# Optimization experiments

Measured on AMD Instinct MI355X. Metric: run time of the kernel, lower is better.

The kernel has to match this reference:

```python
import jax, jax.numpy as jnp
import numpy as np

ND, PD, NH = 256, 128, 8   # node_dim, pair_dim, n_head
HD = ND // NH              # head_dim = 32
N, L = 1, 256


def _inorm(x):
    # InstanceNorm2d (affine=False), x is NHWC: normalize per (N,C) over H,W
    m = jnp.mean(x, axis=(1, 2), keepdims=True)
    v = jnp.var(x, axis=(1, 2), keepdims=True)
    return (x - m) * jax.lax.rsqrt(v + 1e-5)


def _conv3x3(x, w, b):
    # w in torch OIHW layout -> HWIO; stride 1, padding 1 ('SAME')
    y = jax.lax.conv_general_dilated(x, jnp.transpose(w, (2, 3, 1, 0)), (1, 1), 'SAME',
                                     dimension_numbers=('NHWC', 'HWIO', 'NHWC'))
    return y + b


def _lrelu(x):
    return jnp.where(x >= 0, x, 0.01 * x)


def _ln(x, g, b):
    m = jnp.mean(x, axis=-1, keepdims=True)
    v = jnp.var(x, axis=-1, keepdims=True)
    return (x - m) * jax.lax.rsqrt(v + 1e-5) * g + b


def setup_inputs() -> dict:
    key = jax.random.key(0)
    ks = jax.random.split(key, 16)
    rn = lambda k, s: jax.random.normal(k, s, jnp.float32) * 0.02
    return dict(
        x=jax.random.normal(ks[0], (N, L, ND), jnp.float32),
        z=jax.random.normal(ks[1], (N, L, L, PD), jnp.float32),
        plddt=jax.random.uniform(ks[2], (N, L, L, 1), jnp.float32),
        Wq=rn(ks[3], (ND, ND)), Wk=rn(ks[4], (ND, ND)), Wv=rn(ks[5], (ND, ND)),
        Wp2a=rn(ks[6], (NH, PD)),
        conv_a_w=rn(ks[7], (NH, 2 * NH, 3, 3)), conv_a_b=jnp.zeros((NH,), jnp.float32),
        conv_p_w=rn(ks[8], (NH, NH + 1, 3, 3)), conv_p_b=jnp.zeros((NH,), jnp.float32),
        ln1_g=jnp.ones((NH * PD + ND,), jnp.float32), ln1_b=jnp.zeros((NH * PD + ND,), jnp.float32),
        lin1_w=rn(ks[9], (2 * ND, NH * PD + ND)), lin1_b=jnp.zeros((2 * ND,), jnp.float32),
        ln2_g=jnp.ones((2 * ND,), jnp.float32), ln2_b=jnp.zeros((2 * ND,), jnp.float32),
        lin2_w=rn(ks[10], (ND, 2 * ND)), lin2_b=jnp.zeros((ND,), jnp.float32),
        lnf_g=jnp.ones((ND,), jnp.float32), lnf_b=jnp.zeros((ND,), jnp.float32),
        conv_z_w=rn(ks[11], (PD, NH + PD, 3, 3)), conv_z_b=jnp.zeros((PD,), jnp.float32),
    )


def reference(x, z, plddt, Wq, Wk, Wv, Wp2a, conv_a_w, conv_a_b, conv_p_w, conv_p_b,
              ln1_g, ln1_b, lin1_w, lin1_b, ln2_g, ln2_b, lin2_w, lin2_b,
              lnf_g, lnf_b, conv_z_w, conv_z_b):
    n, l, _ = x.shape
    inv_sqrt_hd = np.float32(1.0 / np.sqrt(HD))
    # _node2alpha: per-head QK^T / sqrt(head_dim) -> (N,L,L,H)
    q = (x @ Wq.T).reshape(n, l, NH, HD)
    k = (x @ Wk.T).reshape(n, l, NH, HD)
    v = (x @ Wv.T).reshape(n, l, NH, HD)
    a_node = jnp.einsum('nihd,njhd->nijh', q, k) * inv_sqrt_hd
    # _pair2alpha
    a_pair = z @ Wp2a.T  # (N,L,L,H)
    # conv2dalpha: cat(pair, node) channels-last, InstanceNorm + Conv3x3 + LeakyReLU
    alpha = _lrelu(_conv3x3(_inorm(jnp.concatenate([a_pair, a_node], axis=-1)), conv_a_w, conv_a_b))
    # alpha_mask_plddt
    alpha = _lrelu(_conv3x3(_inorm(jnp.concatenate([alpha, plddt], axis=-1)), conv_p_w, conv_p_b))
    # _node_aggregation: (N,L,H,hd) head-major flatten -> (N,L,node_dim)
    node_from_node = jnp.einsum('nijh,njhd->nihd', alpha, v).reshape(n, l, ND)
    # _pair_aggregation: direct contraction over j (avoids (N,L,L,H,P) blowup)
    node_from_pair = jnp.einsum('nijh,nijp->nihp', alpha, z).reshape(n, l, NH * PD)
    # out_transform: LN -> Linear -> LN -> LeakyReLU -> Linear
    h = jnp.concatenate([node_from_pair, node_from_node], axis=-1)
    h = _ln(h, ln1_g, ln1_b)
    h = _ln(h @ lin1_w.T + lin1_b, ln2_g, ln2_b)
    x_out = _lrelu(h) @ lin2_w.T + lin2_b
    x_new = _ln(x + x_out, lnf_g, lnf_b)
    # alpha2pair
    z_new = _lrelu(_conv3x3(_inorm(jnp.concatenate([z, alpha], axis=-1)), conv_z_w, conv_z_b))
    return x_new, z_new
```

## Files before the change

### kernel.cpp

```cpp
#include <hip/hip_runtime.h>
#include <math.h>

#define LLEN 256
#define NDIM 256
#define NHEAD 8
#define HDIM 32
#define NPIX (LLEN*LLEN)

typedef __bf16 bf16x8 __attribute__((ext_vector_type(8)));
typedef float f32x4 __attribute__((ext_vector_type(4)));

constexpr size_t OFF_Q     = 0;
constexpr size_t OFF_K     = 65536;
constexpr size_t OFF_V     = 131072;
constexpr size_t OFF_CAT16 = 196608;
constexpr size_t OFF_H1B   = 196608;
constexpr size_t OFF_W1B   = 360448;
constexpr size_t OFF_A1    = 1245184;
constexpr size_t OFF_ALPHA = 1769472;
constexpr size_t OFF_AGG   = 2293760;
constexpr size_t OFF_Y     = 2621440;
constexpr size_t OFF_ST16  = 2752512;
constexpr size_t OFF_ST9   = 2752544;
constexpr size_t OFF_ST136 = 2752576;
constexpr size_t OFF_PART  = 2752864;
constexpr size_t OFF_PART2 = 2892128;
constexpr size_t OFF_WZB2  = 3031392;

__device__ inline unsigned short f2b(float x){
  union { float f; unsigned u; } a; a.f = x;
  unsigned r = a.u + 0x7fffu + ((a.u >> 16) & 1u);
  return (unsigned short)(r >> 16);
}

__global__ __launch_bounds__(256) void qkv_kernel(
    const float* __restrict__ x, const float* __restrict__ Wq,
    const float* __restrict__ Wk, const float* __restrict__ Wv,
    float* __restrict__ q, float* __restrict__ k, float* __restrict__ v){
  __shared__ __align__(16) float xs[8][256];
  int t = threadIdx.x;
  int i0 = blockIdx.x * 8;
  int m = blockIdx.y;
  const float* W = (m==0)?Wq:((m==1)?Wk:Wv);
  float* out = (m==0)?q:((m==1)?k:v);
  for (int idx = t; idx < 2048; idx += 256)
    xs[idx>>8][idx&255] = x[(size_t)i0*256 + idx];
  __syncthreads();
  float acc[8];
  #pragma unroll
  for (int r = 0; r < 8; r++) acc[r] = 0.f;
  const float4* wr = (const float4*)(W + (size_t)t*256);
  for (int kk = 0; kk < 64; ++kk){
    float4 w4 = wr[kk];
    #pragma unroll
    for (int r = 0; r < 8; r++){
      float4 xv = ((const float4*)xs[r])[kk];
      acc[r] += w4.x*xv.x + w4.y*xv.y + w4.z*xv.z + w4.w*xv.w;
    }
  }
  #pragma unroll
  for (int r = 0; r < 8; r++) out[(size_t)(i0+r)*256 + t] = acc[r];
}

__global__ __launch_bounds__(256) void cat16v2_kernel(
    const float* __restrict__ z, const float* __restrict__ qb,
    const float* __restrict__ kb, const float* __restrict__ Wp2a,
    float* __restrict__ cat16){
  __shared__ __align__(16) float zs2[32*132];
  __shared__ __align__(16) float ws2[8*132];
  __shared__ __align__(16) float qs2[8*36];
  __shared__ __align__(16) float ks2[32*288];
  int t = threadIdx.x;
  int pix0 = blockIdx.x * 32;
  int i = pix0 >> 8;
  int j0 = pix0 & 255;
  {
    int h = t >> 5, j = t & 31;
    float4 v = *(const float4*)(Wp2a + h*128 + j*4);
    *(float4*)(ws2 + h*132 + j*4) = v;
  }
  if (t < 64){
    int h = t >> 3, d4 = t & 7;
    float4 v = *(const float4*)(qb + (size_t)i*256 + h*32 + d4*4);
    *(float4*)(qs2 + h*36 + d4*4) = v;
  }
  #pragma unroll
  for (int k = 0; k < 4; ++k){
    int idx = t + k*256;
    int pix = idx >> 5, j = idx & 31;
    float4 v = *(const float4*)(z + ((size_t)(pix0 + pix))*128 + j*4);
    *(float4*)(zs2 + pix*132 + j*4) = v;
  }
  #pragma unroll
  for (int k = 0; k < 8; ++k){
    int idx = t + k*256;
    int pix = idx >> 6, rem = idx & 63, h = rem >> 3, d4 = rem & 7;
    float4 v = *(const float4*)(kb + ((size_t)(j0 + pix))*256 + h*32 + d4*4);
    *(float4*)(ks2 + pix*288 + h*36 + d4*4) = v;
  }
  __syncthreads();
  int p8 = t >> 3, h = t & 7;
  const float* zr = zs2 + p8*132;
  const float* wr = ws2 + h*132;
  float ap = 0.f;
  #pragma unroll 8
  for (int j = 0; j < 32; ++j){
    float4 a = *(const float4*)(zr + j*4);
    float4 b = *(const float4*)(wr + j*4);
    ap += a.x*b.x + a.y*b.y + a.z*b.z + a.w*b.w;
  }
  const float* qr = qs2 + h*36;
  const float* kr = ks2 + p8*288 + h*36;
  float an = 0.f;
  #pragma unroll
  for (int d4 = 0; d4 < 8; ++d4){
    float4 a = *(const float4*)(qr + d4*4);
    float4 b = *(const float4*)(kr + d4*4);
    an += a.x*b.x + a.y*b.y + a.z*b.z + a.w*b.w;
  }
  an *= 0.17677669529663689f;
  int pix = pix0 + p8;
  cat16[(size_t)pix*16 + h] = ap;
  cat16[(size_t)pix*16 + 8 + h] = an;
}

__global__ __launch_bounds__(256) void statsA_z_kernel(
    const float* __restrict__ z, float* __restrict__ part, float* __restrict__ part2){
  __shared__ float4 sm[256], sq[256];
  int t = threadIdx.x, b = blockIdx.x;
  int c4 = t & 31, po = t >> 5;
  float4 s = {0,0,0,0}, q = {0,0,0,0};
  for (int g = 0; g < 8; ++g){
    int px = b*64 + po + g*8;
    float4 v = *(const float4*)(z + (size_t)px*128 + c4*4);
    s.x += v.x; s.y += v.y; s.z += v.z; s.w += v.w;
    q.x += v.x*v.x; q.y += v.y*v.y; q.z += v.z*v.z; q.w += v.w*v.w;
  }
  sm[t] = s; sq[t] = q;
  __syncthreads();
  if (t < 32){
    float4 S = sm[t], Q = sq[t];
    for (int p2 = 1; p2 < 8; ++p2){
      float4 a = sm[p2*32 + t], c = sq[p2*32 + t];
      S.x += a.x; S.y += a.y; S.z += a.z; S.w += a.w;
      Q.x += c.x; Q.y += c.y; Q.z += c.z; Q.w += c.w;
    }
    part [(size_t)(t*4+0)*1024 + b] = S.x; part [(size_t)(t*4+1)*1024 + b] = S.y;
    part [(size_t)(t*4+2)*1024 + b] = S.z; part [(size_t)(t*4+3)*1024 + b] = S.w;
    part2[(size_t)(t*4+0)*1024 + b] = Q.x; part2[(size_t)(t*4+1)*1024 + b] = Q.y;
    part2[(size_t)(t*4+2)*1024 + b] = Q.z; part2[(size_t)(t*4+3)*1024 + b] = Q.w;
  }
}

__global__ __launch_bounds__(256) void statsA_16_kernel(
    const float* __restrict__ src, float* __restrict__ part, float* __restrict__ part2){
  __shared__ float4 sm[256], sq[256];
  int t = threadIdx.x, b = blockIdx.x;
  int c4 = t & 3, po = t >> 2;
  float4 s = {0,0,0,0}, q = {0,0,0,0};
  for (int g = 0; g < 4; ++g){
    int px = b*256 + po + g*64;
    float4 v = *(const float4*)(src + (size_t)px*16 + c4*4);
    s.x += v.x; s.y += v.y; s.z += v.z; s.w += v.w;
    q.x += v.x*v.x; q.y += v.y*v.y; q.z += v.z*v.z; q.w += v.w*v.w;
  }
  sm[t] = s; sq[t] = q;
  __syncthreads();
  if (t < 4){
    float4 S = sm[t], Q = sq[t];
    for (int p2 = 1; p2 < 64; ++p2){
      float4 a = sm[p2*4 + t], c = sq[p2*4 + t];
      S.x += a.x; S.y += a.y; S.z += a.z; S.w += a.w;
      Q.x += c.x; Q.y += c.y; Q.z += c.z; Q.w += c.w;
    }
    part [(size_t)(t*4+0)*1024 + b] = S.x; part [(size_t)(t*4+1)*1024 + b] = S.y;
    part [(size_t)(t*4+2)*1024 + b] = S.z; part [(size_t)(t*4+3)*1024 + b] = S.w;
    part2[(size_t)(t*4+0)*1024 + b] = Q.x; part2[(size_t)(t*4+1)*1024 + b] = Q.y;
    part2[(size_t)(t*4+2)*1024 + b] = Q.z; part2[(size_t)(t*4+3)*1024 + b] = Q.w;
  }
}

__global__ __launch_bounds__(256) void statsA_s8_kernel(
    const float* __restrict__ src, float* __restrict__ part, float* __restrict__ part2,
    int coff){
  __shared__ float sm[256], sq[256];
  int t = threadIdx.x, b = blockIdx.x;
  int ch = t & 7, po = t >> 3;
  float s = 0.f, q = 0.f;
  for (int g = 0; g < 8; ++g){
    int px = b*256 + po + g*32;
    float v = src[(size_t)px*8 + ch];
    s += v; q += v*v;
  }
  sm[t] = s; sq[t] = q;
  __syncthreads();
  if (t < 8){
    float S = 0.f, Q = 0.f;
    for (int p2 = 0; p2 < 32; ++p2){ S += sm[p2*8 + t]; Q += sq[p2*8 + t]; }
    part [(size_t)(coff+t)*1024 + b] = S;
    part2[(size_t)(coff+t)*1024 + b] = Q;
  }
}

__device__ inline void block_reduce2(float& s, float& s2, float* red){
  int t = threadIdx.x;
  int lane = t & 63, wv = t >> 6;
  #pragma unroll
  for (int o = 32; o > 0; o >>= 1){ s += __shfl_down(s, o); s2 += __shfl_down(s2, o); }
  __syncthreads();
  if (lane == 0){ red[wv] = s; red[4+wv] = s2; }
  __syncthreads();
  s  = red[0]+red[1]+red[2]+red[3];
  s2 = red[4]+red[5]+red[6]+red[7];
}

__global__ __launch_bounds__(256) void statsA_s1_kernel(
    const float* __restrict__ src, float* __restrict__ part, float* __restrict__ part2,
    int coff){
  __shared__ float red[8];
  int t = threadIdx.x, b = blockIdx.x;
  float v = src[(size_t)b*256 + t];
  float s = v, q = v*v;
  block_reduce2(s, q, red);
  if (t == 0){ part[(size_t)coff*1024 + b] = s; part2[(size_t)coff*1024 + b] = q; }
}

__global__ __launch_bounds__(256) void statsB_kernel(
    const float* __restrict__ part, const float* __restrict__ part2,
    float* __restrict__ st, int C, int csplit, int nb_main, int nb_tail){
  __shared__ float red[8];
  int c = blockIdx.x, t = threadIdx.x;
  int nb = (c < csplit) ? nb_main : nb_tail;
  float s = 0.f, q = 0.f;
  for (int i = t; i < nb; i += 256){ s += part[(size_t)c*1024 + i]; q += part2[(size_t)c*1024 + i]; }
  block_reduce2(s, q, red);
  if (t == 0){
    float m = s * (1.f/NPIX);
    float var = q * (1.f/NPIX) - m*m;
    st[c] = m;
    st[C + c] = rsqrtf(var + 1e-5f);
  }
}

template<int CIN, int COUT>
__global__ __launch_bounds__(256) void conv_small5_kernel(
    const float* __restrict__ A, int Ca, const float* __restrict__ B, int Cb,
    const float* __restrict__ st, const float* __restrict__ w,
    const float* __restrict__ bias, float* __restrict__ out){
  constexpr int WD = 67;
  __shared__ float xn[3][CIN][WD];
  __shared__ float wsm[COUT*CIN*9];
  __shared__ float ms[CIN], isd[CIN], bs[COUT];
  int t = threadIdx.x;
  int i = blockIdx.x >> 2, chb = blockIdx.x & 3;
  int c0 = chb*64;
  if (t < CIN){ ms[t] = st[t]; isd[t] = st[CIN + t]; }
  if (t < COUT) bs[t] = bias[t];
  for (int idx = t; idx < COUT*CIN*9; idx += 256) wsm[idx] = w[idx];
  __syncthreads();
  constexpr int TOT = 66*CIN;
  for (int s = 0; s < 3; ++s){
    int ir = i - 1 + s;
    for (int idx = t; idx < TOT; idx += 256){
      int col = idx / CIN, c = idx - col*CIN;
      int gcol = c0 + col - 1;
      float vv = 0.f;
      if (ir >= 0 && ir < 256 && gcol >= 0 && gcol < 256){
        size_t pix = (size_t)ir*256 + gcol;
        float raw = (c < Ca) ? A[pix*Ca + c] : B[pix*Cb + (c - Ca)];
        vv = (raw - ms[c]) * isd[c];
      }
      xn[s][c][col] = vv;
    }
  }
  __syncthreads();
  int os = t >> 6, tc = t & 63;
  float a0 = bs[os*2], a1 = bs[os*2 + 1];
  #pragma unroll
  for (int kh = 0; kh < 3; ++kh){
    #pragma unroll
    for (int c = 0; c < CIN; ++c){
      float x0 = xn[kh][c][tc];
      float x1 = xn[kh][c][tc + 1];
      float x2 = xn[kh][c][tc + 2];
      const float* w0 = wsm + (((os*2+0)*CIN + c)*3 + kh)*3;
      const float* w1 = wsm + (((os*2+1)*CIN + c)*3 + kh)*3;
      a0 += x0*w0[0] + x1*w0[1] + x2*w0[2];
      a1 += x0*w1[0] + x1*w1[1] + x2*w1[2];
    }
  }
  a0 = (a0 >= 0.f) ? a0 : 0.01f*a0;
  a1 = (a1 >= 0.f) ? a1 : 0.01f*a1;
  float2 v2 = { a0, a1 };
  *(float2*)(out + ((size_t)(i*256 + c0 + tc))*COUT + os*2) = v2;
}

__global__ __launch_bounds__(512) void agg_kernel2(
    const float* __restrict__ alpha, const float* __restrict__ z,
    const float* __restrict__ v, float* __restrict__ agg){
  __shared__ float as[2048];
  __shared__ float pp[256][4];
  __shared__ float np[256];
  int i = blockIdx.x, t = threadIdx.x;
  for (int idx = t; idx < 2048; idx += 512) as[idx] = alpha[(size_t)i*2048 + idx];
  __syncthreads();
  int tt = t & 255, jh = t >> 8;
  int p = tt & 127, hh = tt >> 7;
  const float* zrow = z + (size_t)i*32768 + (size_t)jh*128*128;
  const float* ar0 = as + jh*128*8;
  float a0=0.f, a1=0.f, a2=0.f, a3=0.f;
  for (int j = 0; j < 128; ++j){
    float zv = zrow[j*128 + p];
    const float* ar = ar0 + j*8 + hh*4;
    a0 += ar[0]*zv; a1 += ar[1]*zv; a2 += ar[2]*zv; a3 += ar[3]*zv;
  }
  int h = tt >> 5;
  float an = 0.f;
  const float* vrow = v + (size_t)jh*128*256;
  const float* ah0 = as + jh*128*8;
  for (int j = 0; j < 128; ++j) an += ah0[j*8 + h]*vrow[j*256 + tt];
  if (jh == 1){
    pp[tt][0]=a0; pp[tt][1]=a1; pp[tt][2]=a2; pp[tt][3]=a3; np[tt]=an;
  }
  __syncthreads();
  if (jh == 0){
    a0 += pp[tt][0]; a1 += pp[tt][1]; a2 += pp[tt][2]; a3 += pp[tt][3];
    an += np[tt];
    size_t ob = (size_t)i*1280;
    agg[ob + (hh*4+0)*128 + p] = a0;
    agg[ob + (hh*4+1)*128 + p] = a1;
    agg[ob + (hh*4+2)*128 + p] = a2;
    agg[ob + (hh*4+3)*128 + p] = a3;
    agg[ob + 1024 + tt] = an;
  }
}

__global__ __launch_bounds__(256) void ln1_kernel(
    const float* __restrict__ agg,
    const float* __restrict__ ln1_g, const float* __restrict__ ln1_b,
    unsigned short* __restrict__ h1b){
  __shared__ float red[8];
  int i = blockIdx.x, t = threadIdx.x;
  float v[5], s = 0.f, s2 = 0.f;
  #pragma unroll
  for (int qq = 0; qq < 5; ++qq){
    v[qq] = agg[(size_t)i*1280 + qq*256 + t];
    s += v[qq]; s2 += v[qq]*v[qq];
  }
  block_reduce2(s, s2, red);
  float m = s*(1.f/1280.f), istd = rsqrtf(s2*(1.f/1280.f) - m*m + 1e-5f);
  #pragma unroll
  for (int qq = 0; qq < 5; ++qq){
    int kk = qq*256 + t;
    h1b[(size_t)i*1280 + kk] = f2b((v[qq] - m)*istd*ln1_g[kk] + ln1_b[kk]);
  }
}

__global__ __launch_bounds__(256) void w1_prep(const float* __restrict__ w,
                                               unsigned short* __restrict__ wb){
  int idx = (blockIdx.x*256 + threadIdx.x)*4;
  float4 v = *(const float4*)(w + idx);
  ushort4 u;
  u.x = f2b(v.x); u.y = f2b(v.y); u.z = f2b(v.z); u.w = f2b(v.w);
  *(ushort4*)(wb + idx) = u;
}

__global__ __launch_bounds__(256) void gemm1_kernel(
    const unsigned short* __restrict__ h1b, const unsigned short* __restrict__ w1b,
    const float* __restrict__ lin1_b, float* __restrict__ y){
  int t = threadIdx.x;
  int mb = blockIdx.x & 3, nb = blockIdx.x >> 2;
  int lane = t & 63, w = t >> 6;
  int li = lane & 15, lg = lane >> 4;
  int mh = w & 1, nh = w >> 1;
  int mbase = mb*64 + mh*32, nbase = nb*64 + nh*32;
  f32x4 acc[2][2];
  #pragma unroll
  for (int a = 0; a < 2; ++a)
    #pragma unroll
    for (int b = 0; b < 2; ++b) acc[a][b] = (f32x4){0.f,0.f,0.f,0.f};
  const unsigned short* ar0 = h1b + (size_t)(mbase + li)*1280 + lg*8;
  const unsigned short* ar1 = ar0 + 16*1280;
  const unsigned short* br0 = w1b + (size_t)(nbase + li)*1280 + lg*8;
  const unsigned short* br1 = br0 + 16*1280;
  #pragma unroll 4
  for (int ks = 0; ks < 40; ++ks){
    bf16x8 a0 = *(const bf16x8*)(ar0 + ks*32);
    bf16x8 a1 = *(const bf16x8*)(ar1 + ks*32);
    bf16x8 b0 = *(const bf16x8*)(br0 + ks*32);
    bf16x8 b1 = *(const bf16x8*)(br1 + ks*32);
    acc[0][0] = __builtin_amdgcn_mfma_f32_16x16x32_bf16(a0, b0, acc[0][0], 0,0,0);
    acc[0][1] = __builtin_amdgcn_mfma_f32_16x16x32_bf16(a0, b1, acc[0][1], 0,0,0);
    acc[1][0] = __builtin_amdgcn_mfma_f32_16x16x32_bf16(a1, b0, acc[1][0], 0,0,0);
    acc[1][1] = __builtin_amdgcn_mfma_f32_16x16x32_bf16(a1, b1, acc[1][1], 0,0,0);
  }
  #pragma unroll
  for (int mi = 0; mi < 2; ++mi){
    #pragma unroll
    for (int ni = 0; ni < 2; ++ni){
      int col = nbase + ni*16 + li;
      float bb = lin1_b[col];
      #pragma unroll
      for (int ri = 0; ri < 4; ++ri){
        int row = mbase + mi*16 + lg*4 + ri;
        y[(size_t)row*512 + col] = acc[mi][ni][ri] + bb;
      }
    }
  }
}

__global__ __launch_bounds__(256) void outB_kernel(
    const float* __restrict__ y, const float* __restrict__ x,
    const float* __restrict__ ln2_g, const float* __restrict__ ln2_b,
    const float* __restrict__ lin2_w, const float* __restrict__ lin2_b,
    const float* __restrict__ lnf_g, const float* __restrict__ lnf_b,
    float* __restrict__ xout){
  __shared__ __align__(16) float h2[8][512];
  __shared__ float red[8];
  int t = threadIdx.x;
  int rb = blockIdx.x;
  for (int r = 0; r < 8; ++r){
    int i = rb*8 + r;
    float y0 = y[(size_t)i*512 + t], y1 = y[(size_t)i*512 + 256 + t];
    float s = y0 + y1, s2 = y0*y0 + y1*y1;
    block_reduce2(s, s2, red);
    float m = s*(1.f/512.f), istd = rsqrtf(s2*(1.f/512.f) - m*m + 1e-5f);
    float z0 = (y0 - m)*istd*ln2_g[t] + ln2_b[t];
    float z1 = (y1 - m)*istd*ln2_g[t+256] + ln2_b[t+256];
    h2[r][t]     = (z0 >= 0.f) ? z0 : 0.01f*z0;
    h2[r][t+256] = (z1 >= 0.f) ? z1 : 0.01f*z1;
  }
  __syncthreads();
  float acc[8];
  #pragma unroll
  for (int r = 0; r < 8; ++r) acc[r] = 0.f;
  const float4* wr = (const float4*)(lin2_w + (size_t)t*512);
  for (int kk = 0; kk < 128; ++kk){
    float4 w4 = wr[kk];
    #pragma unroll
    for (int r = 0; r < 8; ++r){
      float4 h = ((const float4*)h2[r])[kk];
      acc[r] += w4.x*h.x + w4.y*h.y + w4.z*h.z + w4.w*h.w;
    }
  }
  float bb = lin2_b[t];
  for (int r = 0; r < 8; ++r){
    int i = rb*8 + r;
    float xr = x[(size_t)i*256 + t] + acc[r] + bb;
    float s = xr, s2 = xr*xr;
    block_reduce2(s, s2, red);
    float m = s*(1.f/256.f), istd = rsqrtf(s2*(1.f/256.f) - m*m + 1e-5f);
    xout[(size_t)i*256 + t] = (xr - m)*istd*lnf_g[t] + lnf_b[t];
  }
}

__global__ __launch_bounds__(256) void wz_prep2(const float* __restrict__ w,
                                                unsigned short* __restrict__ wzb2){
  int idx = blockIdx.x*256 + threadIdx.x;
  if (idx >= 23040) return;
  int lane = idx & 63;
  int f = idx >> 6;
  int k = f % 5; int ft = f / 5; int tap = ft % 9; int ocb = ft / 9;
  int oc = ocb*16 + (lane & 15);
  int chb = k*32 + (lane >> 4)*8;
  unsigned short u[8];
  #pragma unroll
  for (int j = 0; j < 8; ++j){
    int ch = chb + j;
    float vv = (ch < 136) ? w[(size_t)oc*1224 + ch*9 + tap] : 0.f;
    u[j] = f2b(vv);
  }
  uint4 pk;
  pk.x = (unsigned)u[0] | ((unsigned)u[1]<<16);
  pk.y = (unsigned)u[2] | ((unsigned)u[3]<<16);
  pk.z = (unsigned)u[4] | ((unsigned)u[5]<<16);
  pk.w = (unsigned)u[6] | ((unsigned)u[7]<<16);
  *(uint4*)(wzb2 + (size_t)idx*8) = pk;
}

__global__ __launch_bounds__(256) void conv_z4_kernel(
    const float* __restrict__ z, const float* __restrict__ alpha,
    const float* __restrict__ st, const unsigned short* __restrict__ wzb2,
    const float* __restrict__ bias, float* __restrict__ out){
  __shared__ __align__(16) unsigned short xs[6*578*8];
  __shared__ __align__(16) float out32[32*132];
  __shared__ float msp[153], isp[153];
  int t = threadIdx.x;
  int stripe = blockIdx.x & 7, rg = blockIdx.x >> 3;
  int i0 = rg*4, c0 = stripe*32;
  int lane = t & 63, w = t >> 6;
  int li = lane & 15, lg = lane >> 4;
  int wocb = w*2;
  if (t < 153){
    int cq = t/9, j = t - cq*9;
    bool vld = (j < 8);
    int ch = cq*8 + j;
    msp[t] = vld ? st[ch] : 0.f;
    isp[t] = vld ? st[136 + ch] : 0.f;
  }
  __syncthreads();
  for (int it = 0; it < 3; ++it){
    int cidx = t + it*256;
    int col = cidx / 17, cq = cidx - col*17;
    int gcol = c0 + col - 1;
    float mm[8], ss[8];
    #pragma unroll
    for (int j = 0; j < 8; ++j){ mm[j] = msp[cq*9 + j]; ss[j] = isp[cq*9 + j]; }
    if (cidx < 578){
      #pragma unroll
      for (int s = 0; s < 6; ++s){
        int ir = i0 - 1 + s;
        uint4 pk = {0u,0u,0u,0u};
        if (ir >= 0 && ir < 256 && gcol >= 0 && gcol < 256){
          const float* src = (cq < 16) ? (z + ((size_t)ir*256 + gcol)*128 + cq*8)
                                       : (alpha + ((size_t)ir*256 + gcol)*8);
          float4 r0 = *(const float4*)src;
          float4 r1 = *(const float4*)(src + 4);
          unsigned short u0 = f2b((r0.x - mm[0])*ss[0]);
          unsigned short u1 = f2b((r0.y - mm[1])*ss[1]);
          unsigned short u2 = f2b((r0.z - mm[2])*ss[2]);
          unsigned short u3 = f2b((r0.w - mm[3])*ss[3]);
          unsigned short u4 = f2b((r1.x - mm[4])*ss[4]);
          unsigned short u5 = f2b((r1.y - mm[5])*ss[5]);
          unsigned short u6 = f2b((r1.z - mm[6])*ss[6]);
          unsigned short u7 = f2b((r1.w - mm[7])*ss[7]);
          pk.x = (unsigned)u0 | ((unsigned)u1<<16);
          pk.y = (unsigned)u2 | ((unsigned)u3<<16);
          pk.z = (unsigned)u4 | ((unsigned)u5<<16);
          pk.w = (unsigned)u6 | ((unsigned)u7<<16);
        }
        *(uint4*)(xs + ((size_t)(s*578 + cidx))*8) = pk;
      }
    }
  }
  __syncthreads();

  f32x4 acc[4][2][2];
  #pragma unroll
  for (int r = 0; r < 4; ++r)
    #pragma unroll
    for (int m = 0; m < 2; ++m)
      #pragma unroll
      for (int o = 0; o < 2; ++o) acc[r][m][o] = (f32x4){0.f,0.f,0.f,0.f};

  for (int kh = 0; kh < 3; ++kh){
    for (int kw = 0; kw < 3; ++kw){
      int tap = kh*3 + kw;
      bf16x8 wf[5][2];
      #pragma unroll
      for (int k = 0; k < 5; ++k)
        #pragma unroll
        for (int o = 0; o < 2; ++o)
          wf[k][o] = *(const bf16x8*)(wzb2 + (size_t)((((wocb+o)*9 + tap)*5 + k)*64 + lane)*8);
      #pragma unroll
      for (int r = 0; r < 4; ++r){
        const unsigned short* sb = xs + (size_t)(r + kh)*578*8;
        #pragma unroll
        for (int k = 0; k < 5; ++k){
          int cq = (k < 4) ? (k*4 + lg) : 16;
          bf16x8 a0 = *(const bf16x8*)(sb + ((li+kw)*17 + cq)*8);
          bf16x8 a1 = *(const bf16x8*)(sb + ((li+kw+16)*17 + cq)*8);
          acc[r][0][0] = __builtin_amdgcn_mfma_f32_16x16x32_bf16(a0, wf[k][0], acc[r][0][0], 0,0,0);
          acc[r][0][1] = __builtin_amdgcn_mfma_f32_16x16x32_bf16(a0, wf[k][1], acc[r][0][1], 0,0,0);
          acc[r][1][0] = __builtin_amdgcn_mfma_f32_16x16x32_bf16(a1, wf[k][0], acc[r][1][0], 0,0,0);
          acc[r][1][1] = __builtin_amdgcn_mfma_f32_16x16x32_bf16(a1, wf[k][1], acc[r][1][1], 0,0,0);
        }
      }
    }
  }

  float4 b4 = *(const float4*)(bias + (t & 31)*4);
  #pragma unroll
  for (int r = 0; r < 4; ++r){
    if (r > 0) __syncthreads();
    #pragma unroll
    for (int ri = 0; ri < 4; ++ri){
      out32[(lg*4 + ri)*132      + (wocb+0)*16 + li] = acc[r][0][0][ri];
      out32[(lg*4 + ri)*132      + (wocb+1)*16 + li] = acc[r][0][1][ri];
      out32[(16 + lg*4 + ri)*132 + (wocb+0)*16 + li] = acc[r][1][0][ri];
      out32[(16 + lg*4 + ri)*132 + (wocb+1)*16 + li] = acc[r][1][1][ri];
    }
    __syncthreads();
    int i = i0 + r;
    #pragma unroll
    for (int it = 0; it < 4; ++it){
      int px = (t >> 5) + it*8;
      float4 v = *(const float4*)(out32 + px*132 + (t & 31)*4);
      v.x += b4.x; v.y += b4.y; v.z += b4.z; v.w += b4.w;
      v.x = (v.x >= 0.f) ? v.x : 0.01f*v.x;
      v.y = (v.y >= 0.f) ? v.y : 0.01f*v.y;
      v.z = (v.z >= 0.f) ? v.z : 0.01f*v.z;
      v.w = (v.w >= 0.f) ? v.w : 0.01f*v.w;
      *(float4*)(out + ((size_t)(i*256 + c0 + px))*128 + (t & 31)*4) = v;
    }
  }
}

extern "C" void kernel_launch(void* const* d_in, const int* in_sizes, int n_in,
                              void* d_out, int out_size, void* d_ws, size_t ws_size,
                              hipStream_t stream){
  const float* x        = (const float*)d_in[0];
  const float* z        = (const float*)d_in[1];
  const float* plddt    = (const float*)d_in[2];
  const float* Wq       = (const float*)d_in[3];
  const float* Wk       = (const float*)d_in[4];
  const float* Wv       = (const float*)d_in[5];
  const float* Wp2a     = (const float*)d_in[6];
  const float* conv_a_w = (const float*)d_in[7];
  const float* conv_a_b = (const float*)d_in[8];
  const float* conv_p_w = (const float*)d_in[9];
  const float* conv_p_b = (const float*)d_in[10];
  const float* ln1_g    = (const float*)d_in[11];
  const float* ln1_b    = (const float*)d_in[12];
  const float* lin1_w   = (const float*)d_in[13];
  const float* lin1_b   = (const float*)d_in[14];
  const float* ln2_g    = (const float*)d_in[15];
  const float* ln2_b    = (const float*)d_in[16];
  const float* lin2_w   = (const float*)d_in[17];
  const float* lin2_b   = (const float*)d_in[18];
  const float* lnf_g    = (const float*)d_in[19];
  const float* lnf_b    = (const float*)d_in[20];
  const float* conv_z_w = (const float*)d_in[21];
  const float* conv_z_b = (const float*)d_in[22];

  float* ws    = (float*)d_ws;
  float* q     = ws + OFF_Q;
  float* k     = ws + OFF_K;
  float* v     = ws + OFF_V;
  float* cat16 = ws + OFF_CAT16;
  float* a1    = ws + OFF_A1;
  float* alpha = ws + OFF_ALPHA;
  float* agg   = ws + OFF_AGG;
  float* y     = ws + OFF_Y;
  float* st16  = ws + OFF_ST16;
  float* st9   = ws + OFF_ST9;
  float* st136 = ws + OFF_ST136;
  float* part  = ws + OFF_PART;
  float* part2 = ws + OFF_PART2;
  unsigned short* wzb2 = (unsigned short*)(ws + OFF_WZB2);
  unsigned short* h1b  = (unsigned short*)(ws + OFF_H1B);
  unsigned short* w1b  = (unsigned short*)(ws + OFF_W1B);

  float* xout = (float*)d_out;
  float* zout = (float*)d_out + 65536;

  qkv_kernel<<<dim3(32,3), 256, 0, stream>>>(x, Wq, Wk, Wv, q, k, v);
  cat16v2_kernel<<<2048, 256, 0, stream>>>(z, q, k, Wp2a, cat16);
  statsA_16_kernel<<<256, 256, 0, stream>>>(cat16, part, part2);
  statsB_kernel<<<16, 256, 0, stream>>>(part, part2, st16, 16, 16, 256, 256);
  conv_small5_kernel<16,8><<<1024, 256, 0, stream>>>(cat16, 16, (const float*)nullptr, 0,
                                                     st16, conv_a_w, conv_a_b, a1);
  statsA_s8_kernel<<<256, 256, 0, stream>>>(a1, part, part2, 0);
  statsA_s1_kernel<<<256, 256, 0, stream>>>(plddt, part, part2, 8);
  statsB_kernel<<<9, 256, 0, stream>>>(part, part2, st9, 9, 9, 256, 256);
  conv_small5_kernel<9,8><<<1024, 256, 0, stream>>>(a1, 8, plddt, 1,
                                                    st9, conv_p_w, conv_p_b, alpha);
  agg_kernel2<<<256, 512, 0, stream>>>(alpha, z, v, agg);
  w1_prep<<<640, 256, 0, stream>>>(lin1_w, w1b);
  ln1_kernel<<<256, 256, 0, stream>>>(agg, ln1_g, ln1_b, h1b);
  gemm1_kernel<<<32, 256, 0, stream>>>(h1b, w1b, lin1_b, y);
  outB_kernel<<<32, 256, 0, stream>>>(y, x, ln2_g, ln2_b, lin2_w, lin2_b,
                                      lnf_g, lnf_b, xout);
  statsA_z_kernel<<<1024, 256, 0, stream>>>(z, part, part2);
  statsA_s8_kernel<<<256, 256, 0, stream>>>(alpha, part, part2, 128);
  statsB_kernel<<<136, 256, 0, stream>>>(part, part2, st136, 136, 128, 1024, 256);
  wz_prep2<<<90, 256, 0, stream>>>(conv_z_w, wzb2);
  conv_z4_kernel<<<512, 256, 0, stream>>>(z, alpha, st136, wzb2, conv_z_b, zout);
}
```

Measured before the change: 197.3 us.

## Double-buffer conv_z weight loads, store epilogue directly, drop q/k LDS staging

The conv_z kernel now fully unrolls the nine taps and loads the next tap's weight fragments into a second register buffer while the current tap's MFMAs run, so global weight latency is hidden. Its epilogue writes accumulators straight to global memory with bias and LeakyReLU applied, removing the out32 LDS staging and its barriers, at the cost of narrower, less coalesced stores. The cat16 kernel stops staging q and k in shared memory and reads them directly from global/cache, which cuts LDS use and may raise occupancy. Double buffering adds register pressure.

```diff
diff --git a/kernel.cpp b/kernel.cpp
--- a/kernel.cpp
+++ b/kernel.cpp
@@ -62,14 +62,12 @@
   for (int r = 0; r < 8; r++) out[(size_t)(i0+r)*256 + t] = acc[r];
 }
 
-__global__ __launch_bounds__(256) void cat16v2_kernel(
+__global__ __launch_bounds__(256) void cat16v3_kernel(
     const float* __restrict__ z, const float* __restrict__ qb,
     const float* __restrict__ kb, const float* __restrict__ Wp2a,
     float* __restrict__ cat16){
   __shared__ __align__(16) float zs2[32*132];
   __shared__ __align__(16) float ws2[8*132];
-  __shared__ __align__(16) float qs2[8*36];
-  __shared__ __align__(16) float ks2[32*288];
   int t = threadIdx.x;
   int pix0 = blockIdx.x * 32;
   int i = pix0 >> 8;
@@ -79,24 +77,12 @@
     float4 v = *(const float4*)(Wp2a + h*128 + j*4);
     *(float4*)(ws2 + h*132 + j*4) = v;
   }
-  if (t < 64){
-    int h = t >> 3, d4 = t & 7;
-    float4 v = *(const float4*)(qb + (size_t)i*256 + h*32 + d4*4);
-    *(float4*)(qs2 + h*36 + d4*4) = v;
-  }
   #pragma unroll
   for (int k = 0; k < 4; ++k){
     int idx = t + k*256;
     int pix = idx >> 5, j = idx & 31;
     float4 v = *(const float4*)(z + ((size_t)(pix0 + pix))*128 + j*4);
     *(float4*)(zs2 + pix*132 + j*4) = v;
-  }
-  #pragma unroll
-  for (int k = 0; k < 8; ++k){
-    int idx = t + k*256;
-    int pix = idx >> 6, rem = idx & 63, h = rem >> 3, d4 = rem & 7;
-    float4 v = *(const float4*)(kb + ((size_t)(j0 + pix))*256 + h*32 + d4*4);
-    *(float4*)(ks2 + pix*288 + h*36 + d4*4) = v;
   }
   __syncthreads();
   int p8 = t >> 3, h = t & 7;
@@ -109,13 +95,13 @@
     float4 b = *(const float4*)(wr + j*4);
     ap += a.x*b.x + a.y*b.y + a.z*b.z + a.w*b.w;
   }
-  const float* qr = qs2 + h*36;
-  const float* kr = ks2 + p8*288 + h*36;
+  const float* qg = qb + (size_t)i*256 + h*32;
+  const float* kg = kb + (size_t)(j0 + p8)*256 + h*32;
   float an = 0.f;
   #pragma unroll
   for (int d4 = 0; d4 < 8; ++d4){
-    float4 a = *(const float4*)(qr + d4*4);
-    float4 b = *(const float4*)(kr + d4*4);
+    float4 a = *(const float4*)(qg + d4*4);
+    float4 b = *(const float4*)(kg + d4*4);
     an += a.x*b.x + a.y*b.y + a.z*b.z + a.w*b.w;
   }
   an *= 0.17677669529663689f;
@@ -478,12 +464,34 @@
   *(uint4*)(wzb2 + (size_t)idx*8) = pk;
 }
 
-__global__ __launch_bounds__(256) void conv_z4_kernel(
+#define LOADW(WF, TAP) { \
+  _Pragma("unroll") \
+  for (int k_ = 0; k_ < 5; ++k_) \
+    _Pragma("unroll") \
+    for (int o_ = 0; o_ < 2; ++o_) \
+      WF[k_][o_] = *(const bf16x8*)(wzb2 + (size_t)((((wocb+o_)*9 + (TAP))*5 + k_)*64 + lane)*8); }
+
+#define CTAPX(TAP, WF) { \
+  const int kh_ = (TAP)/3, kw_ = (TAP)%3; \
+  _Pragma("unroll") \
+  for (int r_ = 0; r_ < 4; ++r_){ \
+    const unsigned short* sb_ = xs + (size_t)(r_ + kh_)*578*8; \
+    _Pragma("unroll") \
+    for (int k_ = 0; k_ < 5; ++k_){ \
+      int cq_ = (k_ < 4) ? (k_*4 + lg) : 16; \
+      bf16x8 a0_ = *(const bf16x8*)(sb_ + ((li+kw_)*17 + cq_)*8); \
+      bf16x8 a1_ = *(const bf16x8*)(sb_ + ((li+kw_+16)*17 + cq_)*8); \
+      acc[r_][0][0] = __builtin_amdgcn_mfma_f32_16x16x32_bf16(a0_, WF[k_][0], acc[r_][0][0], 0,0,0); \
+      acc[r_][0][1] = __builtin_amdgcn_mfma_f32_16x16x32_bf16(a0_, WF[k_][1], acc[r_][0][1], 0,0,0); \
+      acc[r_][1][0] = __builtin_amdgcn_mfma_f32_16x16x32_bf16(a1_, WF[k_][0], acc[r_][1][0], 0,0,0); \
+      acc[r_][1][1] = __builtin_amdgcn_mfma_f32_16x16x32_bf16(a1_, WF[k_][1], acc[r_][1][1], 0,0,0); \
+    } } }
+
+__global__ __launch_bounds__(256) void conv_z5_kernel(
     const float* __restrict__ z, const float* __restrict__ alpha,
     const float* __restrict__ st, const unsigned short* __restrict__ wzb2,
     const float* __restrict__ bias, float* __restrict__ out){
   __shared__ __align__(16) unsigned short xs[6*578*8];
-  __shared__ __align__(16) float out32[32*132];
   __shared__ float msp[153], isp[153];
   int t = threadIdx.x;
   int stripe = blockIdx.x & 7, rg = blockIdx.x >> 3;
@@ -543,55 +551,36 @@
       #pragma unroll
       for (int o = 0; o < 2; ++o) acc[r][m][o] = (f32x4){0.f,0.f,0.f,0.f};
 
-  for (int kh = 0; kh < 3; ++kh){
-    for (int kw = 0; kw < 3; ++kw){
-      int tap = kh*3 + kw;
-      bf16x8 wf[5][2];
+  bf16x8 wfA[5][2], wfB[5][2];
+  LOADW(wfA, 0);
+  LOADW(wfB, 1); CTAPX(0, wfA);
+  LOADW(wfA, 2); CTAPX(1, wfB);
+  LOADW(wfB, 3); CTAPX(2, wfA);
+  LOADW(wfA, 4); CTAPX(3, wfB);
+  LOADW(wfB, 5); CTAPX(4, wfA);
+  LOADW(wfA, 6); CTAPX(5, wfB);
+  LOADW(wfB, 7); CTAPX(6, wfA);
+  LOADW(wfA, 8); CTAPX(7, wfB);
+  CTAPX(8, wfA);
+
+  float b0 = bias[wocb*16 + li];
+  float b1 = bias[(wocb+1)*16 + li];
+  #pragma unroll
+  for (int r = 0; r < 4; ++r){
+    int i = i0 + r;
+    #pragma unroll
+    for (int m = 0; m < 2; ++m){
       #pragma unroll
-      for (int k = 0; k < 5; ++k)
-        #pragma unroll
-        for (int o = 0; o < 2; ++o)
-          wf[k][o] = *(const bf16x8*)(wzb2 + (size_t)((((wocb+o)*9 + tap)*5 + k)*64 + lane)*8);
-      #pragma unroll
-      for (int r = 0; r < 4; ++r){
-        const unsigned short* sb = xs + (size_t)(r + kh)*578*8;
-        #pragma unroll
-        for (int k = 0; k < 5; ++k){
-          int cq = (k < 4) ? (k*4 + lg) : 16;
-          bf16x8 a0 = *(const bf16x8*)(sb + ((li+kw)*17 + cq)*8);
-          bf16x8 a1 = *(const bf16x8*)(sb + ((li+kw+16)*17 + cq)*8);
-          acc[r][0][0] = __builtin_amdgcn_mfma_f32_16x16x32_bf16(a0, wf[k][0], acc[r][0][0], 0,0,0);
-          acc[r][0][1] = __builtin_amdgcn_mfma_f32_16x16x32_bf16(a0, wf[k][1], acc[r][0][1], 0,0,0);
-          acc[r][1][0] = __builtin_amdgcn_mfma_f32_16x16x32_bf16(a1, wf[k][0], acc[r][1][0], 0,0,0);
-          acc[r][1][1] = __builtin_amdgcn_mfma_f32_16x16x32_bf16(a1, wf[k][1], acc[r][1][1], 0,0,0);
-        }
+      for (int ri = 0; ri < 4; ++ri){
+        int px = m*16 + lg*4 + ri;
+        size_t obase = ((size_t)(i*256 + c0 + px))*128;
+        float v0 = acc[r][m][0][ri] + b0;
+        float v1 = acc[r][m][1][ri] + b1;
+        v0 = (v0 >= 0.f) ? v0 : 0.01f*v0;
+        v1 = (v1 >= 0.f) ? v1 : 0.01f*v1;
+        out[obase + wocb*16 + li]     = v0;
+        out[obase + (wocb+1)*16 + li] = v1;
       }
-    }
-  }
-
-  float4 b4 = *(const float4*)(bias + (t & 31)*4);
-  #pragma unroll
-  for (int r = 0; r < 4; ++r){
-    if (r > 0) __syncthreads();
-    #pragma unroll
-    for (int ri = 0; ri < 4; ++ri){
-      out32[(lg*4 + ri)*132      + (wocb+0)*16 + li] = acc[r][0][0][ri];
-      out32[(lg*4 + ri)*132      + (wocb+1)*16 + li] = acc[r][0][1][ri];
-      out32[(16 + lg*4 + ri)*132 + (wocb+0)*16 + li] = acc[r][1][0][ri];
-      out32[(16 + lg*4 + ri)*132 + (wocb+1)*16 + li] = acc[r][1][1][ri];
-    }
-    __syncthreads();
-    int i = i0 + r;
-    #pragma unroll
-    for (int it = 0; it < 4; ++it){
-      int px = (t >> 5) + it*8;
-      float4 v = *(const float4*)(out32 + px*132 + (t & 31)*4);
-      v.x += b4.x; v.y += b4.y; v.z += b4.z; v.w += b4.w;
-      v.x = (v.x >= 0.f) ? v.x : 0.01f*v.x;
-      v.y = (v.y >= 0.f) ? v.y : 0.01f*v.y;
-      v.z = (v.z >= 0.f) ? v.z : 0.01f*v.z;
-      v.w = (v.w >= 0.f) ? v.w : 0.01f*v.w;
-      *(float4*)(out + ((size_t)(i*256 + c0 + px))*128 + (t & 31)*4) = v;
     }
   }
 }
@@ -645,7 +634,7 @@
   float* zout = (float*)d_out + 65536;
 
   qkv_kernel<<<dim3(32,3), 256, 0, stream>>>(x, Wq, Wk, Wv, q, k, v);
-  cat16v2_kernel<<<2048, 256, 0, stream>>>(z, q, k, Wp2a, cat16);
+  cat16v3_kernel<<<2048, 256, 0, stream>>>(z, q, k, Wp2a, cat16);
   statsA_16_kernel<<<256, 256, 0, stream>>>(cat16, part, part2);
   statsB_kernel<<<16, 256, 0, stream>>>(part, part2, st16, 16, 16, 256, 256);
   conv_small5_kernel<16,8><<<1024, 256, 0, stream>>>(cat16, 16, (const float*)nullptr, 0,
@@ -665,5 +654,5 @@
   statsA_s8_kernel<<<256, 256, 0, stream>>>(alpha, part, part2, 128);
   statsB_kernel<<<136, 256, 0, stream>>>(part, part2, st136, 136, 128, 1024, 256);
   wz_prep2<<<90, 256, 0, stream>>>(conv_z_w, wzb2);
-  conv_z4_kernel<<<512, 256, 0, stream>>>(z, alpha, st136, wzb2, conv_z_b, zout);
-}
+  conv_z5_kernel<<<512, 256, 0, stream>>>(z, alpha, st136, wzb2, conv_z_b, zout);
+}
```

Result: slower. 217.0 us (+10.0%).
